# Performance work log

Hardware: AMD Instinct MI355X
Metric: run time of the kernel (lower is better)

Reference implementation:

```python
import jax, jax.numpy as jnp
import numpy as np

B, SEQ, D = 4, 4096, 64      # batch, sequence length, head dim
BS = 32                      # block_size_sparsity
V = 512                      # relative-info embedding vocabulary
R = SEQ // BS                # block rows per batch


def setup_inputs() -> dict:
    key = jax.random.key(0)
    k1, k2, k3 = jax.random.split(key, 3)
    q = jax.random.normal(k1, (B, SEQ, D), jnp.float32)
    emb = jax.random.normal(k2, (B, V, D), jnp.float32)
    # causal lower-triangular block-sparsity layout -> nonzero indices
    rb, cb = np.tril_indices(R)
    idxs_batch = jnp.asarray(np.repeat(np.arange(B), rb.size), jnp.int32)
    idxs_row = jnp.asarray(np.tile(rb, B), jnp.int32)
    P = B * rb.size  # number of nonzero sparse blocks (= 33024)
    info = jax.random.randint(k3, (P, BS, BS), 0, V, jnp.int32)
    return {"q": q, "emb": emb, "info": info,
            "idxs_batch": idxs_batch, "idxs_row": idxs_row}


def reference(q, emb, info, idxs_batch, idxs_row):
    # out[p,i,j] = <q[b_p, r_p*BS + i, :], emb[b_p, info[p,i,j], :]>
    # Compute dense per-batch scores once, then gather per sparse block.
    scores = jnp.einsum('bmd,bvd->bmv', q, emb)            # [B, SEQ, V]
    rows = idxs_row[:, None] * BS + jnp.arange(BS, dtype=jnp.int32)  # [P, BS]
    out = scores[idxs_batch[:, None, None], rows[:, :, None], info]  # [P, BS, BS]
    return out
```

## Files before the change

kernel.cpp:

```cpp
#include <hip/hip_runtime.h>

#define Bn   4
#define SEQn 4096
#define Dn   64
#define BSn  32
#define Vn   512
#define Rn   128
#define PPB  8256


#define SEP  258
#define QWS  68

#define LOADI(R0, R1, R2, R3, itb)                                        \
  {                                                                       \
    int p0_ = ((itb) + 0) * 4 + sub, p1_ = ((itb) + 1) * 4 + sub;         \
    int p2_ = ((itb) + 2) * 4 + sub, p3_ = ((itb) + 3) * 4 + sub;         \
    R0 = info4[(base + (size_t)(p0_ <= r ? p0_ : 0)) * 256 + t];          \
    R1 = info4[(base + (size_t)(p1_ <= r ? p1_ : 0)) * 256 + t];          \
    R2 = info4[(base + (size_t)(p2_ <= r ? p2_ : 0)) * 256 + t];          \
    R3 = info4[(base + (size_t)(p3_ <= r ? p3_ : 0)) * 256 + t];          \
  }

#define PROC1(RV, pp)                                                     \
  if ((pp) <= r) {                                                        \
    float4 o_;                                                            \
    o_.x = slab[rowoff + RV.x];                                           \
    o_.y = slab[rowoff + RV.y];                                           \
    o_.z = slab[rowoff + RV.z];                                           \
    o_.w = slab[rowoff + RV.w];                                           \
    out4[(base + (size_t)(pp)) * 256 + t] = o_;                           \
  }

#define PROCI(R0, R1, R2, R3, itb)                                        \
  {                                                                       \
    PROC1(R0, ((itb) + 0) * 4 + sub);                                     \
    PROC1(R1, ((itb) + 1) * 4 + sub);                                     \
    PROC1(R2, ((itb) + 2) * 4 + sub);                                     \
    PROC1(R3, ((itb) + 3) * 4 + sub);                                     \
  }

__global__ __launch_bounds__(1024, 4) void fused_kernel(
    const float* __restrict__ q, const float* __restrict__ emb,
    const int* __restrict__ info, float* __restrict__ out)
{
  __shared__ float sq[32 * QWS];
  __shared__ float se[Dn * SEP];
  __shared__ float slab[BSn * Vn];

  const int pair = blockIdx.x;
  const int b    = blockIdx.y;
  const int tid  = threadIdx.x;

  const int sub    = tid >> 8;
  const int t      = tid & 255;
  const int rowoff = (t >> 3) << 9;

  const int rg = tid >> 7;
  const int v2 = tid & 127;

  const int4*   info4 = (const int4*)info;
  float4*       out4  = (float4*)out;
  const float2* se2   = (const float2*)se;
  float2*       slab2 = (float2*)slab;

  for (int s = 0; s < 2; ++s) {
    const int r = s ? (127 - pair) : pair;
    const size_t base = (size_t)b * PPB + (((size_t)r * (r + 1)) >> 1);
    const int NIT = (r + 4) >> 2;

    if (tid < 512) {
      const float4* qs4 = (const float4*)(q + ((size_t)b * SEQn + (size_t)r * BSn) * Dn);
      float4 x = qs4[tid];
      ((float4*)sq)[(tid >> 4) * (QWS / 4) + (tid & 15)] = x;
    }

    int4 A0, A1, A2, A3;
    LOADI(A0, A1, A2, A3, 0);

    for (int hv = 0; hv < 2; ++hv) {
      __syncthreads();
      {
        const float4* es4 = (const float4*)(emb + ((size_t)b * Vn + (size_t)hv * 256) * Dn);
#pragma unroll
        for (int k = 0; k < 4; ++k) {
          int idx = tid + (k << 10);
          float4 x = es4[idx];
          int vp = idx >> 4;
          int d0 = (idx & 15) << 2;
          se[(d0 + 0) * SEP + vp] = x.x;
          se[(d0 + 1) * SEP + vp] = x.y;
          se[(d0 + 2) * SEP + vp] = x.z;
          se[(d0 + 3) * SEP + vp] = x.w;
        }
      }
      __syncthreads();
      float2 a0 = {0.f, 0.f}, a1 = {0.f, 0.f}, a2 = {0.f, 0.f}, a3 = {0.f, 0.f};
      const float* qb = sq + (rg * 4) * QWS;
#pragma unroll
      for (int d0 = 0; d0 < Dn; d0 += 4) {
        float4 Q0 = *(const float4*)(qb + d0);
        float4 Q1 = *(const float4*)(qb + QWS + d0);
        float4 Q2 = *(const float4*)(qb + 2 * QWS + d0);
        float4 Q3 = *(const float4*)(qb + 3 * QWS + d0);
        float2 e0 = se2[(d0 + 0) * (SEP / 2) + v2];
        float2 e1 = se2[(d0 + 1) * (SEP / 2) + v2];
        float2 e2 = se2[(d0 + 2) * (SEP / 2) + v2];
        float2 e3 = se2[(d0 + 3) * (SEP / 2) + v2];
        a0.x += Q0.x * e0.x; a0.y += Q0.x * e0.y;
        a1.x += Q1.x * e0.x; a1.y += Q1.x * e0.y;
        a2.x += Q2.x * e0.x; a2.y += Q2.x * e0.y;
        a3.x += Q3.x * e0.x; a3.y += Q3.x * e0.y;
        a0.x += Q0.y * e1.x; a0.y += Q0.y * e1.y;
        a1.x += Q1.y * e1.x; a1.y += Q1.y * e1.y;
        a2.x += Q2.y * e1.x; a2.y += Q2.y * e1.y;
        a3.x += Q3.y * e1.x; a3.y += Q3.y * e1.y;
        a0.x += Q0.z * e2.x; a0.y += Q0.z * e2.y;
        a1.x += Q1.z * e2.x; a1.y += Q1.z * e2.y;
        a2.x += Q2.z * e2.x; a2.y += Q2.z * e2.y;
        a3.x += Q3.z * e2.x; a3.y += Q3.z * e2.y;
        a0.x += Q0.w * e3.x; a0.y += Q0.w * e3.y;
        a1.x += Q1.w * e3.x; a1.y += Q1.w * e3.y;
        a2.x += Q2.w * e3.x; a2.y += Q2.w * e3.y;
        a3.x += Q3.w * e3.x; a3.y += Q3.w * e3.y;
      }
      {
        int sb = (rg * 4) * 256 + (hv << 7) + v2;
        slab2[sb]       = a0;
        slab2[sb + 256] = a1;
        slab2[sb + 512] = a2;
        slab2[sb + 768] = a3;
      }
    }
    __syncthreads();

    for (int it0 = 0; it0 < NIT; it0 += 8) {
      int4 B0, B1, B2, B3;
      if (it0 + 4 < NIT) LOADI(B0, B1, B2, B3, it0 + 4);
      PROCI(A0, A1, A2, A3, it0);
      if (it0 + 8 < NIT) LOADI(A0, A1, A2, A3, it0 + 8);
      if (it0 + 4 < NIT) PROCI(B0, B1, B2, B3, it0 + 4);
    }
  }
}

extern "C" void kernel_launch(void* const* d_in, const int* in_sizes, int n_in,
                              void* d_out, int out_size, void* d_ws, size_t ws_size,
                              hipStream_t stream) {
  const float* q    = (const float*)d_in[0];
  const float* emb  = (const float*)d_in[1];
  const int*   info = (const int*)d_in[2];
  float* out = (float*)d_out;
  (void)d_ws; (void)ws_size;

  dim3 grid(64, Bn);
  fused_kernel<<<grid, 1024, 0, stream>>>(q, emb, info, out);
}
```

Baseline: 276.1 us.

## Pre-transpose emb in a separate kernel and split blocks into half-row tiles

A small kernel now transposes emb into a d-major workspace, so the main kernel reads E vectors straight from global/L2 instead of staging and transposing them in shared memory. The main kernel drops from 256 blocks of 1024 threads, each handling a row pair, to 1024 blocks of 512 threads, each handling one half (16 rows) of one block-row. This cuts shared memory per block and spreads the triangular workload over many more workgroups. In exchange it adds a second launch and a workspace dependency, and emb is reread from cache by every block.

```diff
diff --git a/kernel.cpp b/kernel.cpp
--- a/kernel.cpp
+++ b/kernel.cpp
@@ -8,9 +8,40 @@
 #define Rn   128
 #define PPB  8256
 
+__global__ __launch_bounds__(256) void transpose_kernel(
+    const float* __restrict__ emb, float* __restrict__ embT)
+{
+  __shared__ float tile[64][65];
+  int b  = blockIdx.x >> 3;
+  int v0 = (blockIdx.x & 7) * 64;
+  int t  = threadIdx.x;
+#pragma unroll
+  for (int k = 0; k < 4; ++k) {
+    int idx = t + 256 * k;
+    int v   = idx >> 4;
+    int d4  = idx & 15;
+    float4 x = ((const float4*)(emb + ((size_t)b * Vn + v0 + v) * Dn))[d4];
+    tile[v][d4 * 4 + 0] = x.x;
+    tile[v][d4 * 4 + 1] = x.y;
+    tile[v][d4 * 4 + 2] = x.z;
+    tile[v][d4 * 4 + 3] = x.w;
+  }
+  __syncthreads();
+#pragma unroll
+  for (int k = 0; k < 4; ++k) {
+    int idx = t + 256 * k;
+    int d   = idx >> 4;
+    int j4  = idx & 15;
+    float4 y;
+    y.x = tile[j4 * 4 + 0][d];
+    y.y = tile[j4 * 4 + 1][d];
+    y.z = tile[j4 * 4 + 2][d];
+    y.w = tile[j4 * 4 + 3][d];
+    ((float4*)(embT + ((size_t)b * Dn + d) * Vn + v0))[j4] = y;
+  }
+}
 
-#define SEP  258
-#define QWS  68
+#define QWS 68
 
 #define LOADI(R0, R1, R2, R3, itb)                                        \
   {                                                                       \
@@ -40,107 +71,88 @@
     PROC1(R3, ((itb) + 3) * 4 + sub);                                     \
   }
 
-__global__ __launch_bounds__(1024, 4) void fused_kernel(
-    const float* __restrict__ q, const float* __restrict__ emb,
+#define FMAK(C)                                                           \
+  Ac0.x += Q0.C * E.x; Ac0.y += Q0.C * E.y;                               \
+  Ac0.z += Q0.C * E.z; Ac0.w += Q0.C * E.w;                               \
+  Ac1.x += Q1.C * E.x; Ac1.y += Q1.C * E.y;                               \
+  Ac1.z += Q1.C * E.z; Ac1.w += Q1.C * E.w;                               \
+  Ac2.x += Q2.C * E.x; Ac2.y += Q2.C * E.y;                               \
+  Ac2.z += Q2.C * E.z; Ac2.w += Q2.C * E.w;                               \
+  Ac3.x += Q3.C * E.x; Ac3.y += Q3.C * E.y;                               \
+  Ac3.z += Q3.C * E.z; Ac3.w += Q3.C * E.w;
+
+__global__ __launch_bounds__(512, 8) void fused_kernel(
+    const float* __restrict__ q, const float* __restrict__ embT,
     const int* __restrict__ info, float* __restrict__ out)
 {
-  __shared__ float sq[32 * QWS];
-  __shared__ float se[Dn * SEP];
-  __shared__ float slab[BSn * Vn];
+  __shared__ float sq[16 * QWS];
+  __shared__ float slab[16 * Vn];
 
-  const int pair = blockIdx.x;
-  const int b    = blockIdx.y;
-  const int tid  = threadIdx.x;
+  const int x  = blockIdx.x;
+  const int b  = x & 3;
+  const int u  = (x >> 2) & 63;
+  const int qd = x >> 8;
+  const int h  = u & 1;
+  const int a  = u >> 1;
+  const int r  = (qd == 0) ? a : (qd == 1) ? (63 - a)
+               : (qd == 2) ? (64 + a) : (127 - a);
 
-  const int sub    = tid >> 8;
-  const int t      = tid & 255;
-  const int rowoff = (t >> 3) << 9;
+  const size_t base = (size_t)b * PPB + (((size_t)r * (r + 1)) >> 1);
+  const int tid = threadIdx.x;
 
-  const int rg = tid >> 7;
-  const int v2 = tid & 127;
+  if (tid < 256) {
+    const float4* qs4 = (const float4*)(q +
+        ((size_t)b * SEQn + (size_t)r * BSn + (size_t)h * 16) * Dn);
+    float4 v = qs4[tid];
+    ((float4*)sq)[(tid >> 4) * (QWS / 4) + (tid & 15)] = v;
+  }
+  __syncthreads();
 
-  const int4*   info4 = (const int4*)info;
-  float4*       out4  = (float4*)out;
-  const float2* se2   = (const float2*)se;
-  float2*       slab2 = (float2*)slab;
+  {
+    const int ig = tid >> 7;
+    const int v0 = (tid & 127) * 4;
+    const float* qb    = sq + (ig * 4) * QWS;
+    const float* ebase = embT + (size_t)b * Dn * Vn + v0;
 
-  for (int s = 0; s < 2; ++s) {
-    const int r = s ? (127 - pair) : pair;
-    const size_t base = (size_t)b * PPB + (((size_t)r * (r + 1)) >> 1);
-    const int NIT = (r + 4) >> 2;
+    float4 Ac0 = {0,0,0,0}, Ac1 = {0,0,0,0}, Ac2 = {0,0,0,0}, Ac3 = {0,0,0,0};
+#pragma unroll
+    for (int d0 = 0; d0 < Dn; d0 += 4) {
+      float4 Q0 = *(const float4*)(qb + d0);
+      float4 Q1 = *(const float4*)(qb + QWS + d0);
+      float4 Q2 = *(const float4*)(qb + 2 * QWS + d0);
+      float4 Q3 = *(const float4*)(qb + 3 * QWS + d0);
+      float4 E;
+      E = *(const float4*)(ebase + (d0 + 0) * Vn);  FMAK(x)
+      E = *(const float4*)(ebase + (d0 + 1) * Vn);  FMAK(y)
+      E = *(const float4*)(ebase + (d0 + 2) * Vn);  FMAK(z)
+      E = *(const float4*)(ebase + (d0 + 3) * Vn);  FMAK(w)
+    }
+    float* sb = slab + (ig * 4) * Vn + v0;
+    *(float4*)(sb)          = Ac0;
+    *(float4*)(sb + Vn)     = Ac1;
+    *(float4*)(sb + 2 * Vn) = Ac2;
+    *(float4*)(sb + 3 * Vn) = Ac3;
+  }
 
-    if (tid < 512) {
-      const float4* qs4 = (const float4*)(q + ((size_t)b * SEQn + (size_t)r * BSn) * Dn);
-      float4 x = qs4[tid];
-      ((float4*)sq)[(tid >> 4) * (QWS / 4) + (tid & 15)] = x;
-    }
+  const int sub    = tid >> 7;
+  const int t7     = tid & 127;
+  const int t      = h * 128 + t7;
+  const int rowoff = (t7 >> 3) << 9;
 
-    int4 A0, A1, A2, A3;
-    LOADI(A0, A1, A2, A3, 0);
+  const int4* info4 = (const int4*)info;
+  float4*     out4  = (float4*)out;
+  const int   NIT   = (r + 4) >> 2;
 
-    for (int hv = 0; hv < 2; ++hv) {
-      __syncthreads();
-      {
-        const float4* es4 = (const float4*)(emb + ((size_t)b * Vn + (size_t)hv * 256) * Dn);
-#pragma unroll
-        for (int k = 0; k < 4; ++k) {
-          int idx = tid + (k << 10);
-          float4 x = es4[idx];
-          int vp = idx >> 4;
-          int d0 = (idx & 15) << 2;
-          se[(d0 + 0) * SEP + vp] = x.x;
-          se[(d0 + 1) * SEP + vp] = x.y;
-          se[(d0 + 2) * SEP + vp] = x.z;
-          se[(d0 + 3) * SEP + vp] = x.w;
-        }
-      }
-      __syncthreads();
-      float2 a0 = {0.f, 0.f}, a1 = {0.f, 0.f}, a2 = {0.f, 0.f}, a3 = {0.f, 0.f};
-      const float* qb = sq + (rg * 4) * QWS;
-#pragma unroll
-      for (int d0 = 0; d0 < Dn; d0 += 4) {
-        float4 Q0 = *(const float4*)(qb + d0);
-        float4 Q1 = *(const float4*)(qb + QWS + d0);
-        float4 Q2 = *(const float4*)(qb + 2 * QWS + d0);
-        float4 Q3 = *(const float4*)(qb + 3 * QWS + d0);
-        float2 e0 = se2[(d0 + 0) * (SEP / 2) + v2];
-        float2 e1 = se2[(d0 + 1) * (SEP / 2) + v2];
-        float2 e2 = se2[(d0 + 2) * (SEP / 2) + v2];
-        float2 e3 = se2[(d0 + 3) * (SEP / 2) + v2];
-        a0.x += Q0.x * e0.x; a0.y += Q0.x * e0.y;
-        a1.x += Q1.x * e0.x; a1.y += Q1.x * e0.y;
-        a2.x += Q2.x * e0.x; a2.y += Q2.x * e0.y;
-        a3.x += Q3.x * e0.x; a3.y += Q3.x * e0.y;
-        a0.x += Q0.y * e1.x; a0.y += Q0.y * e1.y;
-        a1.x += Q1.y * e1.x; a1.y += Q1.y * e1.y;
-        a2.x += Q2.y * e1.x; a2.y += Q2.y * e1.y;
-        a3.x += Q3.y * e1.x; a3.y += Q3.y * e1.y;
-        a0.x += Q0.z * e2.x; a0.y += Q0.z * e2.y;
-        a1.x += Q1.z * e2.x; a1.y += Q1.z * e2.y;
-        a2.x += Q2.z * e2.x; a2.y += Q2.z * e2.y;
-        a3.x += Q3.z * e2.x; a3.y += Q3.z * e2.y;
-        a0.x += Q0.w * e3.x; a0.y += Q0.w * e3.y;
-        a1.x += Q1.w * e3.x; a1.y += Q1.w * e3.y;
-        a2.x += Q2.w * e3.x; a2.y += Q2.w * e3.y;
-        a3.x += Q3.w * e3.x; a3.y += Q3.w * e3.y;
-      }
-      {
-        int sb = (rg * 4) * 256 + (hv << 7) + v2;
-        slab2[sb]       = a0;
-        slab2[sb + 256] = a1;
-        slab2[sb + 512] = a2;
-        slab2[sb + 768] = a3;
-      }
-    }
-    __syncthreads();
+  int4 ivA0, ivA1, ivA2, ivA3;
+  LOADI(ivA0, ivA1, ivA2, ivA3, 0);
+  __syncthreads();
 
-    for (int it0 = 0; it0 < NIT; it0 += 8) {
-      int4 B0, B1, B2, B3;
-      if (it0 + 4 < NIT) LOADI(B0, B1, B2, B3, it0 + 4);
-      PROCI(A0, A1, A2, A3, it0);
-      if (it0 + 8 < NIT) LOADI(A0, A1, A2, A3, it0 + 8);
-      if (it0 + 4 < NIT) PROCI(B0, B1, B2, B3, it0 + 4);
-    }
+  for (int it0 = 0; it0 < NIT; it0 += 8) {
+    int4 ivB0, ivB1, ivB2, ivB3;
+    if (it0 + 4 < NIT) LOADI(ivB0, ivB1, ivB2, ivB3, it0 + 4);
+    PROCI(ivA0, ivA1, ivA2, ivA3, it0);
+    if (it0 + 8 < NIT) LOADI(ivA0, ivA1, ivA2, ivA3, it0 + 8);
+    if (it0 + 4 < NIT) PROCI(ivB0, ivB1, ivB2, ivB3, it0 + 4);
   }
 }
 
@@ -150,9 +162,9 @@
   const float* q    = (const float*)d_in[0];
   const float* emb  = (const float*)d_in[1];
   const int*   info = (const int*)d_in[2];
-  float* out = (float*)d_out;
-  (void)d_ws; (void)ws_size;
+  float* out  = (float*)d_out;
+  float* embT = (float*)d_ws;
 
-  dim3 grid(64, Bn);
-  fused_kernel<<<grid, 1024, 0, stream>>>(q, emb, info, out);
+  transpose_kernel<<<32, 256, 0, stream>>>(emb, embT);
+  fused_kernel<<<1024, 512, 0, stream>>>(q, embT, info, out);
 }
```

New measurement: 296.6 us. 7.4% more time.
